# Performance work log

Measured on AMD Instinct MI355X. Metric: run time of the kernel, lower is better.

## Reference

```python
import jax, jax.numpy as jnp
import numpy as np

BN_EPS = 1e-5
L2_EPS = 1e-12


def setup_inputs() -> dict:
    key = jax.random.key(0)
    ks = jax.random.split(key, 4)
    B, C, H, W = 16, 384, 56, 56
    x = jax.random.normal(ks[0], (B, C, H, W), dtype=jnp.float32)
    w_qkv = jax.random.normal(ks[1], (3 * C, C), dtype=jnp.float32) * (1.0 / np.sqrt(C))
    b_qkv = jnp.zeros((3 * C,), dtype=jnp.float32)
    w_proj = jax.random.normal(ks[2], (C, C), dtype=jnp.float32) * (1.0 / np.sqrt(C))
    b_proj = jnp.zeros((C,), dtype=jnp.float32)
    bn_gamma = jnp.ones((C,), dtype=jnp.float32)
    bn_beta = jnp.zeros((C,), dtype=jnp.float32)
    bn_mean = jnp.zeros((C,), dtype=jnp.float32)
    bn_var = jnp.ones((C,), dtype=jnp.float32)
    temperature = jnp.ones((1,), dtype=jnp.float32)
    return {"x": x, "w_qkv": w_qkv, "b_qkv": b_qkv, "w_proj": w_proj,
            "b_proj": b_proj, "bn_gamma": bn_gamma, "bn_beta": bn_beta,
            "bn_mean": bn_mean, "bn_var": bn_var, "temperature": temperature}


def _l2norm_lastdim(t):
    # F.normalize(t, dim=-1): divide by max(||t||_2, eps)
    n = jnp.sqrt(jnp.sum(t * t, axis=-1, keepdims=True))
    return t / jnp.maximum(n, L2_EPS)


def reference(x, w_qkv, b_qkv, w_proj, b_proj, bn_gamma, bn_beta, bn_mean, bn_var, temperature):
    B, C, H, W = x.shape
    N = H * W
    # BatchNorm2d (eval mode, running stats)
    scale = bn_gamma / jnp.sqrt(bn_var + BN_EPS)          # [C]
    shift = bn_beta - bn_mean * scale                     # [C]
    xn = x * scale[None, :, None, None] + shift[None, :, None, None]
    # 1x1 conv qkv: C -> 3C, operate on flattened spatial [B, C, N]
    xn_f = xn.reshape(B, C, N)
    qkv = jnp.einsum('oc,bcn->bon', w_qkv, xn_f) + b_qkv[None, :, None]  # [B,3C,N]
    q, k, v = qkv[:, :C], qkv[:, C:2 * C], qkv[:, 2 * C:]
    q = _l2norm_lastdim(q)                                # [B,C,N]
    k = _l2norm_lastdim(k)
    # channel-transposed attention: [B,C,C]
    logits = jnp.einsum('bcn,bdn->bcd', q, k) * temperature[0]
    attn = jax.nn.softmax(logits, axis=-1)
    fused = jnp.einsum('bcd,bdn->bcn', attn, v)           # [B,C,N]
    # 1x1 proj conv + residual
    out = jnp.einsum('oc,bcn->bon', w_proj, fused) + b_proj[None, :, None]
    return x + out.reshape(B, C, H, W)
```

## Files before the change

kernel.cpp:

```cpp
#include <hip/hip_runtime.h>

#define BATCH 16
#define CCH   384
#define NSP   3136
#define NSPP  3200

typedef unsigned short u16;
typedef float  f32x4  __attribute__((ext_vector_type(4)));
typedef __bf16 bf16x8 __attribute__((ext_vector_type(8)));

__device__ __forceinline__ float bf2f(u16 u) {
  union { unsigned int i; float f; } v; v.i = ((unsigned int)u) << 16; return v.f;
}
__device__ __forceinline__ u16 f2bf(float f) {
  union { float f; unsigned int i; } v; v.f = f;
  unsigned int i = v.i;
  return (u16)((i + 0x7fffu + ((i >> 16) & 1u)) >> 16);
}
__device__ __forceinline__ float rdf(const void* p, long i, bool bf) {
  return bf ? bf2f(((const u16*)p)[i]) : ((const float*)p)[i];
}

__device__ __forceinline__ void gload_lds16(const u16* g, u16* l) {
  __builtin_amdgcn_global_load_lds(
      (const __attribute__((address_space(1))) void*)g,
      (__attribute__((address_space(3))) void*)l, 16, 0, 0);
}

__global__ void transpose_kernel(const void* __restrict__ x, u16* __restrict__ xt,
                                 const u16* __restrict__ probe) {
  const bool bf = (probe[0] == 0x3F80u);
  __shared__ float Ls[32 * 65];
  const int t = threadIdx.x;
  const int n0 = blockIdx.x * 64, c0 = blockIdx.y * 32, b = blockIdx.z;
  if (n0 >= NSP) {
    const int n_l = t >> 2, c8 = (t & 3) * 8;
    uint4 zq = make_uint4(0, 0, 0, 0);
    *(uint4*)(xt + ((long)b * NSPP + n0 + n_l) * CCH + c0 + c8) = zq;
    return;
  }
  {
    const int c_l = t >> 3, n8 = (t & 7) * 8;
    const long src = ((long)b * CCH + c0 + c_l) * NSP + n0 + n8;
    float v[8];
    if (bf) {
      union { uint4 q; u16 e[8]; } u; u.q = *(const uint4*)((const u16*)x + src);
      #pragma unroll
      for (int i = 0; i < 8; i++) v[i] = bf2f(u.e[i]);
    } else {
      float4 a = *(const float4*)((const float*)x + src);
      float4 c = *(const float4*)((const float*)x + src + 4);
      v[0]=a.x; v[1]=a.y; v[2]=a.z; v[3]=a.w; v[4]=c.x; v[5]=c.y; v[6]=c.z; v[7]=c.w;
    }
    #pragma unroll
    for (int i = 0; i < 8; i++) Ls[c_l * 65 + n8 + i] = v[i];
  }
  __syncthreads();
  {
    const int n_l = t >> 2, c8 = (t & 3) * 8;
    union { uint4 q; u16 e[8]; } o;
    #pragma unroll
    for (int i = 0; i < 8; i++) o.e[i] = f2bf(Ls[(c8 + i) * 65 + n_l]);
    *(uint4*)(xt + ((long)b * NSPP + n0 + n_l) * CCH + c0 + c8) = o.q;
  }
}

__global__ void prep_kernel(const void* __restrict__ w_qkv, const void* __restrict__ b_qkv,
                            const void* __restrict__ gamma, const void* __restrict__ beta,
                            const void* __restrict__ mean,  const void* __restrict__ var,
                            const void* __restrict__ b_proj, const void* __restrict__ w_proj,
                            u16* __restrict__ w_eff, float* __restrict__ b_eff,
                            float* __restrict__ bproj_f,
                            unsigned* __restrict__ w2qk, unsigned* __restrict__ wp2,
                            u16* __restrict__ wvT, float* __restrict__ szero,
                            const u16* __restrict__ probe) {
  const bool bf = (probe[0] == 0x3F80u);
  __shared__ float s_scale[CCH], s_shift[CCH];
  const int tid = threadIdx.x;
  const int o = blockIdx.x;
  if (o < 72) {
    szero[o * 256 + tid] = 0.f;
    szero[o * 256 + 128 + tid] = 0.f;
  }
  for (int c = tid; c < CCH; c += 128) {
    float g = rdf(gamma, c, bf), bt = rdf(beta, c, bf);
    float mn = rdf(mean, c, bf), vr = rdf(var, c, bf);
    float sc = g * rsqrtf(vr + 1e-5f);
    s_scale[c] = sc; s_shift[c] = bt - mn * sc;
  }
  __syncthreads();
  float part = 0.f;
  for (int c = tid; c < CCH; c += 128) {
    float w = rdf(w_qkv, (long)o * CCH + c, bf);
    u16 wv = f2bf(w * s_scale[c]);
    w_eff[(long)o * CCH + c] = wv;
    if (o < 768) w2qk[(long)o * CCH + c] = (unsigned)wv | ((unsigned)wv << 16);
    else         wvT[(long)c * CCH + (o - 768)] = wv;
    part += w * s_shift[c];
  }
  for (int off = 32; off > 0; off >>= 1) part += __shfl_down(part, off, 64);
  __shared__ float s_part[2];
  if ((tid & 63) == 0) s_part[tid >> 6] = part;
  __syncthreads();
  if (tid == 0) b_eff[o] = rdf(b_qkv, o, bf) + s_part[0] + s_part[1];
  if (o < CCH) {
    for (int c = tid; c < CCH; c += 128) {
      u16 pv = f2bf(rdf(w_proj, (long)o * CCH + c, bf));
      wp2[(long)o * CCH + c] = (unsigned)pv | ((unsigned)pv << 16);
    }
  }
  if (o == 0) {
    for (int c = tid; c < CCH; c += 128) bproj_f[c] = rdf(b_proj, c, bf);
  }
}

template<int BM, int BN, int WGM, int WGN, int OUTM, bool BIASM, bool RES,
         int NCHK, bool EPIL, bool SUMX, int SRC>
__launch_bounds__(256)
__global__ void gemm_nt(const u16* __restrict__ A, const u16* __restrict__ B,
                        void* __restrict__ Cv,
                        const float* __restrict__ biasm,
                        const void* __restrict__ resv,
                        int K, int lda, int ldb, int ldc,
                        long sA, long sB, long sC, long sRes,
                        int zb, int nLim, int sBM,
                        float* __restrict__ qns, const u16* __restrict__ epW,
                        float* __restrict__ sxp,
                        const u16* __restrict__ probe) {
  constexpr int WM = BM / WGM, WN = BN / WGN;
  constexpr int FM = WM / 16,  FN = WN / 16;
  constexpr int NA = BM / 32,  NB = BN / 32;
  constexpr bool BOUNCE = (OUTM == 1 || OUTM == 2) && (BM == BN) && (WGN == 2);
  constexpr int RPF = WGM * 16;
  constexpr int LBS = BN + 4;
  constexpr int SM_STAGE  = (BM + BN) * 128;
  constexpr int SM_BOUNCE = BOUNCE ? RPF * LBS * 4 : 0;
  constexpr int SM_BYTES  = SM_STAGE > SM_BOUNCE ? SM_STAGE : SM_BOUNCE;
  __shared__ __align__(16) char smem[SM_BYTES];
  u16* As = (u16*)smem;
  u16* Bs = (u16*)(smem + BM * 128);
  const bool f32io = (probe[0] != 0x3F80u);
  const int tid = threadIdx.x, wave = tid >> 6, lane = tid & 63;
  const int quad = lane >> 4, l16 = lane & 15;
  const int wm = wave / WGN, wn = wave % WGN;
  const int z = blockIdx.z;
  const u16* A0 = A; const u16* B0 = B;
  A += z * sA; B += z * sB;
  const float* Af = (SRC == 1) ? ((const float*)A0 + z * sA) : nullptr;
  const float* Bf = (SRC == 1) ? ((const float*)B0 + z * sB) : nullptr;
  const long cOff = (long)(zb + z) * sC;
  const long rOff = (long)(zb + z) * sRes;

  const int gx = gridDim.x;
  const int tot = gx * gridDim.y;
  const int wg = blockIdx.y * gx + blockIdx.x;
  const int qq = tot >> 3, rr = tot & 7;
  const int xcd = wg & 7, idx = wg >> 3;
  const int nid = (xcd < rr ? xcd * (qq + 1) : rr * (qq + 1) + (xcd - rr) * qq) + idx;
  const int m0 = (nid % gx) * BM, n0 = (nid / gx) * BN;

  long aoff[NA]; long boff[NB];
  #pragma unroll
  for (int p = 0; p < NA; p++) {
    int u = tid + p * 256, r = u >> 3, k8 = u & 7;
    aoff[p] = (long)(m0 + r) * lda + ((k8 ^ (r & 7)) << 3);
  }
  #pragma unroll
  for (int p = 0; p < NB; p++) {
    int u = tid + p * 256, r = u >> 3, k8 = u & 7;
    boff[p] = (long)(n0 + r) * ldb + ((k8 ^ (r & 7)) << 3);
  }

  f32x4 acc[FM][FN] = {};
  float rs[FM] = {};

  auto compute_tile = [&]() {
    #pragma unroll
    for (int tt = 0; tt < 2; tt++) {
      bf16x8 af[FM], bfr[FN];
      #pragma unroll
      for (int f = 0; f < FM; f++) {
        int r = wm * WM + f * 16 + l16;
        af[f] = *(const bf16x8*)&As[r * 64 + (((tt * 4 + quad) ^ (l16 & 7)) << 3)];
      }
      #pragma unroll
      for (int g = 0; g < FN; g++) {
        int r = wn * WN + g * 16 + l16;
        bfr[g] = *(const bf16x8*)&Bs[r * 64 + (((tt * 4 + quad) ^ (l16 & 7)) << 3)];
      }
      if (SUMX) {
        if (n0 == 0 && wn == 0) {
          #pragma unroll
          for (int f = 0; f < FM; f++)
            #pragma unroll
            for (int j = 0; j < 8; j++) rs[f] += (float)af[f][j];
        }
      }
      #pragma unroll
      for (int f = 0; f < FM; f++)
        #pragma unroll
        for (int g = 0; g < FN; g++)
          acc[f][g] = __builtin_amdgcn_mfma_f32_16x16x32_bf16(af[f], bfr[g], acc[f][g], 0, 0, 0);
    }
  };

  const int nt = K >> 6;
  if (SRC == 1 && f32io) {
    for (int t = 0; t < nt; t++) {
      #pragma unroll
      for (int p = 0; p < NA; p++) {
        const float* g = Af + aoff[p] + (long)t * 64;
        float4 lo = *(const float4*)g, hi = *(const float4*)(g + 4);
        uint4 q;
        asm("v_cvt_pk_bf16_f32 %0, %1, %2" : "=v"(q.x) : "v"(lo.x), "v"(lo.y));
        asm("v_cvt_pk_bf16_f32 %0, %1, %2" : "=v"(q.y) : "v"(lo.z), "v"(lo.w));
        asm("v_cvt_pk_bf16_f32 %0, %1, %2" : "=v"(q.z) : "v"(hi.x), "v"(hi.y));
        asm("v_cvt_pk_bf16_f32 %0, %1, %2" : "=v"(q.w) : "v"(hi.z), "v"(hi.w));
        *(uint4*)&As[(size_t)(tid + p * 256) * 8] = q;
      }
      #pragma unroll
      for (int p = 0; p < NB; p++) {
        const float* g = Bf + boff[p] + (long)t * 64;
        float4 lo = *(const float4*)g, hi = *(const float4*)(g + 4);
        uint4 q;
        asm("v_cvt_pk_bf16_f32 %0, %1, %2" : "=v"(q.x) : "v"(lo.x), "v"(lo.y));
        asm("v_cvt_pk_bf16_f32 %0, %1, %2" : "=v"(q.y) : "v"(lo.z), "v"(lo.w));
        asm("v_cvt_pk_bf16_f32 %0, %1, %2" : "=v"(q.z) : "v"(hi.x), "v"(hi.y));
        asm("v_cvt_pk_bf16_f32 %0, %1, %2" : "=v"(q.w) : "v"(hi.z), "v"(hi.w));
        *(uint4*)&Bs[(size_t)(tid + p * 256) * 8] = q;
      }
      __syncthreads();
      compute_tile();
      __syncthreads();
    }
  } else {
    for (int t = 0; t < nt; t++) {
      #pragma unroll
      for (int p = 0; p < NA; p++)
        gload_lds16(A + aoff[p] + (long)t * 64, &As[(p * 256 + wave * 64) * 8]);
      #pragma unroll
      for (int p = 0; p < NB; p++)
        gload_lds16(B + boff[p] + (long)t * 64, &Bs[(p * 256 + wave * 64) * 8]);
      __syncthreads();
      compute_tile();
      __syncthreads();
    }
  }

  if (SUMX) {
    if (n0 == 0 && wn == 0) {
      #pragma unroll
      for (int f = 0; f < FM; f++) {
        float r = rs[f];
        r += __shfl_xor(r, 16, 64);
        r += __shfl_xor(r, 32, 64);
        if (quad == 0) atomicAdd(sxp + (long)z * CCH + m0 + wm * WM + f * 16 + l16, r);
      }
    }
  }

  if (BOUNCE) {
    float* Lb = (float*)smem;
    #pragma unroll
    for (int f = 0; f < FM; f++) {
      #pragma unroll
      for (int g = 0; g < FN; g++)
        #pragma unroll
        for (int reg = 0; reg < 4; reg++) {
          float v = acc[f][g][reg];
          if (BIASM) v += biasm[(long)(zb + z) * sBM + m0 + wm * WM + f * 16 + quad * 4 + reg];
          Lb[(wm * 16 + quad * 4 + reg) * LBS + wn * WN + g * 16 + l16] = v;
        }
      __syncthreads();
      {
        const int tr = tid >> 3;
        const int cb = (tid & 7) * (BN / 8);
        const int mm = m0 + (tr >> 4) * WM + f * 16 + (tr & 15);
        const long rowBase = (long)mm * ldc;
        #pragma unroll
        for (int j = 0; j < BN / 32; j++) {
          const int nn = n0 + cb + j * 4;
          const bool live = (NCHK != 2) || (nn < nLim);
          if (live) {
            float4 v = *(const float4*)&Lb[tr * LBS + cb + j * 4];
            if (RES) {
              if (f32io) {
                float4 r = *(const float4*)&((const float*)resv)[rOff + rowBase + nn];
                v.x += r.x; v.y += r.y; v.z += r.z; v.w += r.w;
              } else {
                const u16* rp = (const u16*)resv + rOff + rowBase + nn;
                v.x += bf2f(rp[0]); v.y += bf2f(rp[1]); v.z += bf2f(rp[2]); v.w += bf2f(rp[3]);
              }
            }
            if (OUTM == 1 || f32io) {
              *(float4*)&((float*)Cv)[cOff + rowBase + nn] = v;
            } else {
              ushort4 o4 = { f2bf(v.x), f2bf(v.y), f2bf(v.z), f2bf(v.w) };
              *(ushort4*)((u16*)Cv + cOff + rowBase + nn) = o4;
            }
          }
        }
      }
      __syncthreads();
    }
  } else {
    #pragma unroll
    for (int f = 0; f < FM; f++) {
      #pragma unroll
      for (int reg = 0; reg < 4; reg++) {
        const int mm = m0 + wm * WM + f * 16 + quad * 4 + reg;
        float s2 = 0.f;
        #pragma unroll
        for (int g = 0; g < FN; g++) {
          int nn = n0 + wn * WN + g * 16 + l16;
          float v = acc[f][g][reg];
          if (BIASM) v += biasm[(long)(zb + z) * sBM + mm];
          long off = (long)mm * ldc + nn;
          bool live = true;
          if (NCHK == 2) live = (nn < nLim);
          if (NCHK == 3) live = (mm < nLim);
          if (RES && live) {
            long ro = rOff + off;
            v += f32io ? ((const float*)resv)[ro] : bf2f(((const u16*)resv)[ro]);
          }
          if (EPIL) s2 += v * bf2f(epW[(long)mm * CCH + nn]);
          if (OUTM == 1) {
            ((float*)Cv)[cOff + off] = v;
          } else if (OUTM == 2) {
            if (live) {
              if (f32io) ((float*)Cv)[cOff + off] = v;
              else       ((u16*)Cv)[cOff + off]   = f2bf(v);
            }
          } else if (OUTM == 4) {
            if (live) {
              u16 hi = f2bf(v);
              u16 lo = f2bf(v - bf2f(hi));
              ((unsigned*)Cv)[cOff + off] = (unsigned)hi | ((unsigned)lo << 16);
            }
          } else {
            if (live) ((u16*)Cv)[cOff + off] = f2bf(v);
          }
        }
        if (EPIL) {
          s2 += __shfl_xor(s2, 1, 16);
          s2 += __shfl_xor(s2, 2, 16);
          s2 += __shfl_xor(s2, 4, 16);
          s2 += __shfl_xor(s2, 8, 16);
          if (l16 == 0) atomicAdd(qns + (long)(zb + z) * 768 + mm, s2);
        }
      }
    }
  }
}

__global__ void ugemv_kernel(const u16* __restrict__ w_eff, const float* __restrict__ sx,
                             float* __restrict__ u) {
  const int m = blockIdx.x * 4 + (threadIdx.x >> 6), l = threadIdx.x & 63;
  const int b = blockIdx.y;
  float s = 0.f;
  for (int k = l; k < CCH; k += 64) s += bf2f(w_eff[(long)m * CCH + k]) * sx[b * CCH + k];
  for (int off = 32; off > 0; off >>= 1) s += __shfl_down(s, off, 64);
  if (l == 0) u[b * 768 + m] = s;
}

__global__ void cgemv_kernel(const unsigned* __restrict__ wp2, const float* __restrict__ av,
                             const float* __restrict__ bproj, float* __restrict__ cvec) {
  const int o = blockIdx.x, b = blockIdx.y, l = threadIdx.x;
  float s = 0.f;
  for (int c = l; c < CCH; c += 64)
    s += bf2f((u16)(wp2[(long)o * CCH + c] & 0xffffu)) * av[b * CCH + c];
  for (int off = 32; off > 0; off >>= 1) s += __shfl_down(s, off, 64);
  if (l == 0) cvec[b * CCH + o] = s + bproj[o];
}

__global__ void softmax_kernel(const float* __restrict__ Lg, const float* __restrict__ qn2,
                               const float* __restrict__ u, const float* __restrict__ beff,
                               const void* __restrict__ temp,
                               u16* __restrict__ attn, float* __restrict__ av,
                               const u16* __restrict__ probe) {
  const bool bfm = (probe[0] == 0x3F80u);
  const int c = blockIdx.x, b = blockIdx.y, tid = threadIdx.x;
  const float* row = Lg + ((long)b * CCH + c) * CCH;
  const float beq = beff[c], uq = u[b * 768 + c];
  const float qn = qn2[b * 768 + c] + 2.f * beq * uq + 3136.f * beq * beq;
  const float rq = 1.f / fmaxf(sqrtf(fmaxf(qn, 0.f)), 1e-12f);
  const float T = rdf(temp, 0, bfm);
  float v[3]; float mx = -1e30f;
  #pragma unroll
  for (int j = 0; j < 3; j++) {
    int d = tid + j * 128;
    float bek = beff[384 + d], uk = u[b * 768 + 384 + d];
    float kn = qn2[b * 768 + 384 + d] + 2.f * bek * uk + 3136.f * bek * bek;
    float rd = 1.f / fmaxf(sqrtf(fmaxf(kn, 0.f)), 1e-12f);
    float lg = row[d] + uq * bek + beq * uk + 3136.f * beq * bek;
    v[j] = lg * rq * rd * T;
    mx = fmaxf(mx, v[j]);
  }
  for (int off = 32; off > 0; off >>= 1) mx = fmaxf(mx, __shfl_down(mx, off, 64));
  __shared__ float sm[2];
  if ((tid & 63) == 0) sm[tid >> 6] = mx;
  __syncthreads();
  mx = fmaxf(sm[0], sm[1]);
  float s = 0.f;
  #pragma unroll
  for (int j = 0; j < 3; j++) { v[j] = __expf(v[j] - mx); s += v[j]; }
  for (int off = 32; off > 0; off >>= 1) s += __shfl_down(s, off, 64);
  __shared__ float ss[2];
  if ((tid & 63) == 0) ss[tid >> 6] = s;
  __syncthreads();
  s = ss[0] + ss[1];
  const float inv = 1.f / s;
  float avp = 0.f;
  u16* arow = attn + ((long)b * CCH + c) * CCH;
  #pragma unroll
  for (int j = 0; j < 3; j++) {
    float p = v[j] * inv;
    arow[tid + j * 128] = f2bf(p);
    avp += p * beff[768 + tid + j * 128];
  }
  for (int off = 32; off > 0; off >>= 1) avp += __shfl_down(avp, off, 64);
  __shared__ float sa[2];
  if ((tid & 63) == 0) sa[tid >> 6] = avp;
  __syncthreads();
  if (tid == 0) av[b * CCH + c] = sa[0] + sa[1];
}

extern "C" void kernel_launch(void* const* d_in, const int* in_sizes, int n_in,
                              void* d_out, int out_size, void* d_ws, size_t ws_size,
                              hipStream_t stream) {
  const void* x      = d_in[0];
  const void* w_qkv  = d_in[1];
  const void* b_qkv  = d_in[2];
  const void* w_proj = d_in[3];
  const void* b_proj = d_in[4];
  const void* gamma  = d_in[5];
  const void* beta   = d_in[6];
  const void* mean   = d_in[7];
  const void* var    = d_in[8];
  const void* temp   = d_in[9];
  const u16* probe = (const u16*)gamma;

  const size_t SZ_XT   = (size_t)BATCH * NSPP * CCH * 2;
  const size_t SZ_WEFF = (size_t)1152 * CCH * 2;
  const size_t SZ_W2QK = (size_t)768 * CCH * 4;
  const size_t SZ_WP2  = (size_t)CCH * CCH * 4;
  const size_t SZ_WVT  = (size_t)CCH * CCH * 2;
  const size_t SZ_BEFF = (size_t)1152 * 4;
  const size_t SZ_BPRJ = (size_t)CCH * 4;
  const size_t SZ_U    = (size_t)BATCH * 768 * 4;
  const size_t SZ_AV   = (size_t)BATCH * CCH * 4;
  const size_t SZ_CV   = (size_t)BATCH * CCH * 4;
  const size_t SZ_MM   = (size_t)BATCH * CCH * CCH;

  char* ws = (char*)d_ws;
  u16*      xt    = (u16*)ws;      ws += SZ_XT;
  u16*      w_eff = (u16*)ws;      ws += SZ_WEFF;
  unsigned* w2qk  = (unsigned*)ws; ws += SZ_W2QK;
  unsigned* wp2   = (unsigned*)ws; ws += SZ_WP2;
  u16*      wvT   = (u16*)ws;      ws += SZ_WVT;
  float*    b_eff = (float*)ws;    ws += SZ_BEFF;
  float*    bproj = (float*)ws;    ws += SZ_BPRJ;
  float*    sx    = (float*)ws;    ws += (size_t)BATCH * CCH * 4;
  float*    qn2   = (float*)ws;    ws += (size_t)BATCH * 768 * 4;
  float*    u     = (float*)ws;    ws += SZ_U;
  float*    av    = (float*)ws;    ws += SZ_AV;
  float*    cvec  = (float*)ws;    ws += SZ_CV;
  unsigned* Gs    = (unsigned*)ws; ws += SZ_MM * 4;
  unsigned* Ts    = (unsigned*)ws; ws += SZ_MM * 4;
  float*    Lg    = (float*)ws;    ws += SZ_MM * 4;
  u16*      attn  = (u16*)ws;      ws += SZ_MM * 2;
  unsigned* RTs   = (unsigned*)ws; ws += SZ_MM * 4;
  u16*      Mb    = (u16*)ws;      ws += SZ_MM * 2;

  const long sXB = (long)CCH * NSP;
  const long sMM = (long)CCH * CCH;
  const long sM2 = (long)CCH * 768;

  prep_kernel<<<dim3(1152), dim3(128), 0, stream>>>(
      w_qkv, b_qkv, gamma, beta, mean, var, b_proj, w_proj,
      w_eff, b_eff, bproj, w2qk, wp2, wvT, sx, probe);

  gemm_nt<128, 128, 2, 2, 4, false, false, 0, false, true, 1>
      <<<dim3(3, 3, BATCH), dim3(256), 0, stream>>>(
      (const u16*)x, (const u16*)x, Gs, nullptr, nullptr,
      NSP, NSP, NSP, CCH, sXB, sXB, sMM, 0L,
      0, 0, 0, nullptr, nullptr, sx, probe);

  ugemv_kernel<<<dim3(192, BATCH), dim3(256), 0, stream>>>(w_eff, sx, u);

  gemm_nt<96, 96, 2, 2, 4, false, false, 3, true, false, 0>
      <<<dim3(8, 4, BATCH), dim3(256), 0, stream>>>(
      (const u16*)w2qk, (const u16*)Gs, Ts, nullptr, nullptr,
      768, 768, 768, CCH, 0L, sM2, sMM, 0L,
      0, CCH, 0, qn2, w_eff, nullptr, probe);

  gemm_nt<96, 96, 2, 2, 1, false, false, 0, false, false, 0>
      <<<dim3(4, 4, BATCH), dim3(256), 0, stream>>>(
      (const u16*)Ts, (const u16*)w2qk + (long)384 * 768, Lg, nullptr, nullptr,
      768, 768, 768, CCH, sM2, 0L, sMM, 0L,
      0, 0, 0, nullptr, nullptr, nullptr, probe);

  softmax_kernel<<<dim3(CCH, BATCH), dim3(128), 0, stream>>>(
      Lg, qn2, u, b_eff, temp, attn, av, probe);

  gemm_nt<96, 96, 2, 2, 4, false, false, 0, false, false, 0>
      <<<dim3(4, 4, BATCH), dim3(256), 0, stream>>>(
      wvT, attn, RTs, nullptr, nullptr,
      CCH, CCH, CCH, CCH, 0L, sMM, sMM, 0L,
      0, 0, 0, nullptr, nullptr, nullptr, probe);

  cgemv_kernel<<<dim3(CCH, BATCH), dim3(64), 0, stream>>>(wp2, av, bproj, cvec);

  gemm_nt<96, 96, 2, 2, 0, false, false, 0, false, false, 0>
      <<<dim3(4, 4, BATCH), dim3(256), 0, stream>>>(
      (const u16*)wp2, (const u16*)RTs, Mb, nullptr, nullptr,
      768, 768, 768, CCH, 0L, sM2, sMM, 0L,
      0, 0, 0, nullptr, nullptr, nullptr, probe);

  transpose_kernel<<<dim3(NSPP / 64, CCH / 32, BATCH), dim3(256), 0, stream>>>(
      x, xt, probe);

  gemm_nt<128, 128, 2, 2, 2, true, true, 2, false, false, 0>
      <<<dim3(3, 25, BATCH), dim3(256), 0, stream>>>(
      Mb, xt, d_out, cvec, x,
      CCH, CCH, CCH, NSP, sMM, (long)NSPP * CCH, (long)CCH * NSP, (long)CCH * NSP,
      0, NSP, CCH, nullptr, nullptr, nullptr, probe);
}
```

Baseline: 383.9 us.

## Split-K and symmetry skip for Gram GEMM, fuse reduction with ugemv

The X·Xᵀ Gram GEMM now splits K into 7 chunks and skips upper-triangular tiles, so it launches far more blocks than the previous 144. Each block writes an fp32 partial into a new Gp workspace. A new kernel sums the partials, mirrors the symmetric tiles, and packs the result into the hi/lo bf16 format. The same kernel also does the u GEMV. This trades better CU occupancy for extra partial-sum memory traffic and one more reduction pass. The SUMX row-sum path under split-K also needs to accumulate correctly across chunks.

```diff
diff --git a/kernel.cpp b/kernel.cpp
--- a/kernel.cpp
+++ b/kernel.cpp
@@ -4,6 +4,7 @@
 #define CCH   384
 #define NSP   3136
 #define NSPP  3200
+#define GKS   7
 
 typedef unsigned short u16;
 typedef float  f32x4  __attribute__((ext_vector_type(4)));
@@ -115,7 +116,7 @@
 }
 
 template<int BM, int BN, int WGM, int WGN, int OUTM, bool BIASM, bool RES,
-         int NCHK, bool EPIL, bool SUMX, int SRC>
+         int NCHK, bool EPIL, bool SUMX, bool SYMM, int SRC, int KS>
 __launch_bounds__(256)
 __global__ void gemm_nt(const u16* __restrict__ A, const u16* __restrict__ B,
                         void* __restrict__ Cv,
@@ -130,7 +131,7 @@
   constexpr int WM = BM / WGM, WN = BN / WGN;
   constexpr int FM = WM / 16,  FN = WN / 16;
   constexpr int NA = BM / 32,  NB = BN / 32;
-  constexpr bool BOUNCE = (OUTM == 1 || OUTM == 2) && (BM == BN) && (WGN == 2);
+  constexpr bool BOUNCE = (OUTM == 2) && (BM == BN) && (WGN == 2);
   constexpr int RPF = WGM * 16;
   constexpr int LBS = BN + 4;
   constexpr int SM_STAGE  = (BM + BN) * 128;
@@ -143,7 +144,8 @@
   const int tid = threadIdx.x, wave = tid >> 6, lane = tid & 63;
   const int quad = lane >> 4, l16 = lane & 15;
   const int wm = wave / WGN, wn = wave % WGN;
-  const int z = blockIdx.z;
+  int z = blockIdx.z, kc = 0;
+  if (KS > 1) { kc = z % KS; z /= KS; }
   const u16* A0 = A; const u16* B0 = B;
   A += z * sA; B += z * sB;
   const float* Af = (SRC == 1) ? ((const float*)A0 + z * sA) : nullptr;
@@ -158,17 +160,20 @@
   const int xcd = wg & 7, idx = wg >> 3;
   const int nid = (xcd < rr ? xcd * (qq + 1) : rr * (qq + 1) + (xcd - rr) * qq) + idx;
   const int m0 = (nid % gx) * BM, n0 = (nid / gx) * BN;
+  if (SYMM && n0 > m0) return;
+
+  const int kLen = K / KS, kBeg = kc * kLen;
 
   long aoff[NA]; long boff[NB];
   #pragma unroll
   for (int p = 0; p < NA; p++) {
     int u = tid + p * 256, r = u >> 3, k8 = u & 7;
-    aoff[p] = (long)(m0 + r) * lda + ((k8 ^ (r & 7)) << 3);
+    aoff[p] = (long)(m0 + r) * lda + kBeg + ((k8 ^ (r & 7)) << 3);
   }
   #pragma unroll
   for (int p = 0; p < NB; p++) {
     int u = tid + p * 256, r = u >> 3, k8 = u & 7;
-    boff[p] = (long)(n0 + r) * ldb + ((k8 ^ (r & 7)) << 3);
+    boff[p] = (long)(n0 + r) * ldb + kBeg + ((k8 ^ (r & 7)) << 3);
   }
 
   f32x4 acc[FM][FN] = {};
@@ -204,7 +209,7 @@
     }
   };
 
-  const int nt = K >> 6;
+  const int nt = kLen >> 6;
   if (SRC == 1 && f32io) {
     for (int t = 0; t < nt; t++) {
       #pragma unroll
@@ -292,7 +297,7 @@
                 v.x += bf2f(rp[0]); v.y += bf2f(rp[1]); v.z += bf2f(rp[2]); v.w += bf2f(rp[3]);
               }
             }
-            if (OUTM == 1 || f32io) {
+            if (f32io) {
               *(float4*)&((float*)Cv)[cOff + rowBase + nn] = v;
             } else {
               ushort4 o4 = { f2bf(v.x), f2bf(v.y), f2bf(v.z), f2bf(v.w) };
@@ -325,7 +330,7 @@
           }
           if (EPIL) s2 += v * bf2f(epW[(long)mm * CCH + nn]);
           if (OUTM == 1) {
-            ((float*)Cv)[cOff + off] = v;
+            ((float*)Cv)[cOff + off + ((KS > 1) ? (long)kc * sRes : 0L)] = v;
           } else if (OUTM == 2) {
             if (live) {
               if (f32io) ((float*)Cv)[cOff + off] = v;
@@ -353,14 +358,28 @@
   }
 }
 
-__global__ void ugemv_kernel(const u16* __restrict__ w_eff, const float* __restrict__ sx,
-                             float* __restrict__ u) {
-  const int m = blockIdx.x * 4 + (threadIdx.x >> 6), l = threadIdx.x & 63;
-  const int b = blockIdx.y;
-  float s = 0.f;
-  for (int k = l; k < CCH; k += 64) s += bf2f(w_eff[(long)m * CCH + k]) * sx[b * CCH + k];
-  for (int off = 32; off > 0; off >>= 1) s += __shfl_down(s, off, 64);
-  if (l == 0) u[b * 768 + m] = s;
+__global__ void gred_ugemv_kernel(const float* __restrict__ Gp, unsigned* __restrict__ Gs,
+                                  const u16* __restrict__ w_eff, const float* __restrict__ sx,
+                                  float* __restrict__ u) {
+  const int b = blockIdx.y, bx = blockIdx.x, tid = threadIdx.x;
+  if (bx < 576) {
+    const int idx = bx * 256 + tid;
+    const int r = idx / CCH, c = idx % CCH;
+    const long e = ((r >> 7) >= (c >> 7)) ? ((long)r * CCH + c) : ((long)c * CCH + r);
+    const long base = (long)b * GKS * (CCH * CCH);
+    float s = 0.f;
+    #pragma unroll
+    for (int k = 0; k < GKS; k++) s += Gp[base + (long)k * (CCH * CCH) + e];
+    u16 hi = f2bf(s);
+    u16 lo = f2bf(s - bf2f(hi));
+    Gs[(long)b * (CCH * CCH) + idx] = (unsigned)hi | ((unsigned)lo << 16);
+  } else {
+    const int m = (bx - 576) * 4 + (tid >> 6), l = tid & 63;
+    float s = 0.f;
+    for (int k = l; k < CCH; k += 64) s += bf2f(w_eff[(long)m * CCH + k]) * sx[b * CCH + k];
+    for (int off = 32; off > 0; off >>= 1) s += __shfl_down(s, off, 64);
+    if (l == 0) u[b * 768 + m] = s;
+  }
 }
 
 __global__ void cgemv_kernel(const unsigned* __restrict__ wp2, const float* __restrict__ av,
@@ -471,6 +490,7 @@
   u16*      attn  = (u16*)ws;      ws += SZ_MM * 2;
   unsigned* RTs   = (unsigned*)ws; ws += SZ_MM * 4;
   u16*      Mb    = (u16*)ws;      ws += SZ_MM * 2;
+  float*    Gp    = (float*)ws;
 
   const long sXB = (long)CCH * NSP;
   const long sMM = (long)CCH * CCH;
@@ -480,21 +500,22 @@
       w_qkv, b_qkv, gamma, beta, mean, var, b_proj, w_proj,
       w_eff, b_eff, bproj, w2qk, wp2, wvT, sx, probe);
 
-  gemm_nt<128, 128, 2, 2, 4, false, false, 0, false, true, 1>
-      <<<dim3(3, 3, BATCH), dim3(256), 0, stream>>>(
-      (const u16*)x, (const u16*)x, Gs, nullptr, nullptr,
-      NSP, NSP, NSP, CCH, sXB, sXB, sMM, 0L,
+  gemm_nt<128, 128, 2, 2, 1, false, false, 0, false, true, true, 1, GKS>
+      <<<dim3(3, 3, BATCH * GKS), dim3(256), 0, stream>>>(
+      (const u16*)x, (const u16*)x, Gp, nullptr, nullptr,
+      NSP, NSP, NSP, CCH, sXB, sXB, (long)GKS * sMM, sMM,
       0, 0, 0, nullptr, nullptr, sx, probe);
 
-  ugemv_kernel<<<dim3(192, BATCH), dim3(256), 0, stream>>>(w_eff, sx, u);
-
-  gemm_nt<96, 96, 2, 2, 4, false, false, 3, true, false, 0>
+  gred_ugemv_kernel<<<dim3(768, BATCH), dim3(256), 0, stream>>>(
+      Gp, Gs, w_eff, sx, u);
+
+  gemm_nt<96, 96, 2, 2, 4, false, false, 3, true, false, false, 0, 1>
       <<<dim3(8, 4, BATCH), dim3(256), 0, stream>>>(
       (const u16*)w2qk, (const u16*)Gs, Ts, nullptr, nullptr,
       768, 768, 768, CCH, 0L, sM2, sMM, 0L,
       0, CCH, 0, qn2, w_eff, nullptr, probe);
 
-  gemm_nt<96, 96, 2, 2, 1, false, false, 0, false, false, 0>
+  gemm_nt<96, 96, 2, 2, 1, false, false, 0, false, false, false, 0, 1>
       <<<dim3(4, 4, BATCH), dim3(256), 0, stream>>>(
       (const u16*)Ts, (const u16*)w2qk + (long)384 * 768, Lg, nullptr, nullptr,
       768, 768, 768, CCH, sM2, 0L, sMM, 0L,
@@ -503,7 +524,7 @@
   softmax_kernel<<<dim3(CCH, BATCH), dim3(128), 0, stream>>>(
       Lg, qn2, u, b_eff, temp, attn, av, probe);
 
-  gemm_nt<96, 96, 2, 2, 4, false, false, 0, false, false, 0>
+  gemm_nt<96, 96, 2, 2, 4, false, false, 0, false, false, false, 0, 1>
       <<<dim3(4, 4, BATCH), dim3(256), 0, stream>>>(
       wvT, attn, RTs, nullptr, nullptr,
       CCH, CCH, CCH, CCH, 0L, sMM, sMM, 0L,
@@ -511,7 +532,7 @@
 
   cgemv_kernel<<<dim3(CCH, BATCH), dim3(64), 0, stream>>>(wp2, av, bproj, cvec);
 
-  gemm_nt<96, 96, 2, 2, 0, false, false, 0, false, false, 0>
+  gemm_nt<96, 96, 2, 2, 0, false, false, 0, false, false, false, 0, 1>
       <<<dim3(4, 4, BATCH), dim3(256), 0, stream>>>(
       (const u16*)wp2, (const u16*)RTs, Mb, nullptr, nullptr,
       768, 768, 768, CCH, 0L, sM2, sMM, 0L,
@@ -520,7 +541,7 @@
   transpose_kernel<<<dim3(NSPP / 64, CCH / 32, BATCH), dim3(256), 0, stream>>>(
       x, xt, probe);
 
-  gemm_nt<128, 128, 2, 2, 2, true, true, 2, false, false, 0>
+  gemm_nt<128, 128, 2, 2, 2, true, true, 2, false, false, false, 0, 1>
       <<<dim3(3, 25, BATCH), dim3(256), 0, stream>>>(
       Mb, xt, d_out, cvec, x,
       CCH, CCH, CCH, NSP, sMM, (long)NSPP * CCH, (long)CCH * NSP, (long)CCH * NSP,
```

Measured after the change: 370.1 us. 1.04x faster.
